# Kernel tuning notes

Measured on AMD Instinct MI355X. Metric: run time of the kernel, lower is better.

Reference implementation:

```python
import jax, jax.numpy as jnp
import numpy as np

ALPHA = 0.2  # LeakyReLU negative slope (init arg `alpha`)
N, F_IN, F_OUT = 8192, 512, 256


def setup_inputs() -> dict:
    key = jax.random.key(0)
    k1, k2, k3, k4 = jax.random.split(key, 4)
    x = jax.random.normal(k1, (N, F_IN), dtype=jnp.float32)
    adj = jax.random.randint(k2, (N, N), 0, 2, dtype=jnp.int32)
    W = jax.random.normal(k3, (F_IN, F_OUT), dtype=jnp.float32) * (1.0 / np.sqrt(F_IN))
    a = jax.random.normal(k4, (2 * F_OUT, 1), dtype=jnp.float32) * (1.0 / np.sqrt(F_IN))
    return {"x": x, "adj": adj, "W": W, "a": a}


def reference(x, adj, W, a):
    h = x @ W  # [N, F_OUT]
    f_out = W.shape[1]
    # e[i,j] = LeakyReLU(a1 . h_i + a2 . h_j); computed without the O(N^2*2F) concat
    f1 = h @ a[:f_out, 0]   # [N]
    f2 = h @ a[f_out:, 0]   # [N]
    s = f1[:, None] + f2[None, :]  # [N, N]
    e = jnp.where(s >= 0, s, ALPHA * s)
    # Faithful to the source bug: -9e15 * zeros_like == zeros, so masked entries are 0.0
    att = jnp.where(adj > 0, e, jnp.zeros((), dtype=e.dtype))
    att = jax.nn.softmax(att, axis=1)
    # dropout is identity in eval mode
    h_prime = att @ h  # [N, F_OUT]
    return jax.nn.elu(h_prime)  # concat=True branch
```

## Files before the change

### kernel.cpp

```cpp
#include <hip/hip_runtime.h>
#include <stdint.h>

#define NN 8192
#define FIN 512
#define FOUT 256
#define ALPHA 0.2f
#define KSPLIT 4

typedef float f32x4 __attribute__((ext_vector_type(4)));
typedef short s16x8 __attribute__((ext_vector_type(8)));

__device__ __forceinline__ uint16_t f2bf(float f) {
  union { float f; uint32_t u; } v; v.f = f;
  uint32_t u = v.u + 0x7fffu + ((v.u >> 16) & 1u);
  return (uint16_t)(u >> 16);
}

__global__ __launch_bounds__(256) void k_wa(const float* __restrict__ W,
                                            const float* __restrict__ a,
                                            float* __restrict__ wa1, float* __restrict__ wa2) {
  __shared__ float a1[256], a2[256];
  int tid = threadIdx.x;
  a1[tid] = a[tid];
  a2[tid] = a[tid + 256];
  __syncthreads();
  int m = blockIdx.x * 256 + tid;
  const float* wrow = W + (size_t)m * FOUT;
  float s1 = 0.f, s2 = 0.f;
  for (int k = 0; k < FOUT; k += 4) {
    f32x4 v = *(const f32x4*)(wrow + k);
#pragma unroll
    for (int i = 0; i < 4; i++) {
      s1 += v[i] * a1[k + i];
      s2 += v[i] * a2[k + i];
    }
  }
  wa1[m] = s1; wa2[m] = s2;
}

__global__ __launch_bounds__(256) void k_f1f2(const float* __restrict__ x,
                                              const float* __restrict__ wa1,
                                              const float* __restrict__ wa2,
                                              float* __restrict__ f1, float* __restrict__ f2) {
  __shared__ float s1[512], s2[512];
  int tid = threadIdx.x;
  s1[tid] = wa1[tid]; s1[tid + 256] = wa1[tid + 256];
  s2[tid] = wa2[tid]; s2[tid + 256] = wa2[tid + 256];
  __syncthreads();
  int w = tid >> 6, l = tid & 63;
  int row = blockIdx.x * 4 + w;
  const float* xr = x + (size_t)row * FIN + l * 8;
  f32x4 v0 = *(const f32x4*)xr;
  f32x4 v1 = *(const f32x4*)(xr + 4);
  int kb = l * 8;
  float d1 = 0.f, d2 = 0.f;
#pragma unroll
  for (int i = 0; i < 4; i++) {
    d1 += v0[i] * s1[kb + i] + v1[i] * s1[kb + 4 + i];
    d2 += v0[i] * s2[kb + i] + v1[i] * s2[kb + 4 + i];
  }
#pragma unroll
  for (int off = 32; off; off >>= 1) {
    d1 += __shfl_down(d1, off);
    d2 += __shfl_down(d2, off);
  }
  if (l == 0) { f1[row] = d1; f2[row] = d2; }
}

__global__ __launch_bounds__(256) void k_prep_wt(const float* __restrict__ W,
                                                 uint16_t* __restrict__ wt) {
  int idx = blockIdx.x * 256 + threadIdx.x;
  int f  = idx >> 7;
  int k4 = (idx & 127) * 4;
  ushort4 o;
  o.x = f2bf(W[(size_t)(k4 + 0) * FOUT + f]);
  o.y = f2bf(W[(size_t)(k4 + 1) * FOUT + f]);
  o.z = f2bf(W[(size_t)(k4 + 2) * FOUT + f]);
  o.w = f2bf(W[(size_t)(k4 + 3) * FOUT + f]);
  *(ushort4*)(wt + (size_t)f * FIN + k4) = o;
}

__global__ __launch_bounds__(256, 2) void k_gemm_h(const float* __restrict__ x,
                                                   const uint16_t* __restrict__ wt,
                                                   uint16_t* __restrict__ h) {
  __shared__ uint16_t Xs[64][40];
  __shared__ uint16_t Ws[128][40];
  int i0 = blockIdx.x * 64;
  int f0 = blockIdx.y * 128;
  int tid = threadIdx.x;
  int w = tid >> 6, l = tid & 63;
  int wr = w >> 1, wc = w & 1;
  int q = l >> 4, r16 = l & 15;
  f32x4 acc[2][4];
#pragma unroll
  for (int a = 0; a < 2; a++)
#pragma unroll
    for (int b = 0; b < 4; b++) acc[a][b] = (f32x4)0.f;

  int srow = tid >> 2, sch = tid & 3;
  for (int k0 = 0; k0 < FIN; k0 += 32) {
    const float* xp = x + (size_t)(i0 + srow) * FIN + k0 + sch * 8;
    f32x4 u0 = *(const f32x4*)xp;
    f32x4 u1 = *(const f32x4*)(xp + 4);
    uint4 pk;
    pk.x = (uint32_t)f2bf(u0[0]) | ((uint32_t)f2bf(u0[1]) << 16);
    pk.y = (uint32_t)f2bf(u0[2]) | ((uint32_t)f2bf(u0[3]) << 16);
    pk.z = (uint32_t)f2bf(u1[0]) | ((uint32_t)f2bf(u1[1]) << 16);
    pk.w = (uint32_t)f2bf(u1[2]) | ((uint32_t)f2bf(u1[3]) << 16);
    *(uint4*)(&Xs[srow][sch * 8]) = pk;
#pragma unroll
    for (int r = 0; r < 2; r++) {
      int idx = tid + r * 256;
      int rr = idx >> 2, cc = idx & 3;
      uint4 vw = *(const uint4*)(wt + (size_t)(f0 + rr) * FIN + k0 + cc * 8);
      *(uint4*)(&Ws[rr][cc * 8]) = vw;
    }
    __syncthreads();
    s16x8 A[2], B[4];
#pragma unroll
    for (int a = 0; a < 2; a++) A[a] = *(const s16x8*)(&Xs[wr * 32 + a * 16 + r16][q * 8]);
#pragma unroll
    for (int b = 0; b < 4; b++) B[b] = *(const s16x8*)(&Ws[wc * 64 + b * 16 + r16][q * 8]);
#pragma unroll
    for (int a = 0; a < 2; a++)
#pragma unroll
      for (int b = 0; b < 4; b++)
        acc[a][b] = __builtin_amdgcn_mfma_f32_16x16x32_bf16(A[a], B[b], acc[a][b], 0, 0, 0);
    __syncthreads();
  }
#pragma unroll
  for (int a = 0; a < 2; a++)
#pragma unroll
    for (int b = 0; b < 4; b++)
#pragma unroll
      for (int reg = 0; reg < 4; reg++) {
        int row = i0 + wr * 32 + a * 16 + q * 4 + reg;
        int col = f0 + wc * 64 + b * 16 + r16;
        h[(size_t)row * FOUT + col] = f2bf(acc[a][b][reg]);
      }
}

__global__ __launch_bounds__(256) void k_transpose(const uint16_t* __restrict__ h,
                                                   uint16_t* __restrict__ ht) {
  __shared__ uint16_t T[64][72];
  int i0 = blockIdx.x * 64, f0 = blockIdx.y * 64;
  int tid = threadIdx.x;
#pragma unroll
  for (int p = 0; p < 2; p++) {
    int idx = tid + p * 256;
    int r = idx >> 3, c8 = idx & 7;
    uint4 v = *(const uint4*)(h + (size_t)(i0 + r) * FOUT + f0 + c8 * 8);
    *(uint4*)(&T[r][c8 * 8]) = v;
  }
  __syncthreads();
#pragma unroll
  for (int p = 0; p < 2; p++) {
    int idx = tid + p * 256;
    int fr = idx >> 3, ic8 = idx & 7;
    s16x8 v;
#pragma unroll
    for (int j = 0; j < 8; j++) v[j] = (short)T[ic8 * 8 + j][fr];
    *(s16x8*)(ht + (size_t)(f0 + fr) * NN + i0 + ic8 * 8) = v;
  }
}

__global__ __launch_bounds__(256) void k_zero(float* __restrict__ l_arr) {
  l_arr[blockIdx.x * 256 + threadIdx.x] = 0.f;
}

__global__ __launch_bounds__(256, 2) void k_att(const int* __restrict__ adj,
                                                const uint16_t* __restrict__ ht,
                                                const float* __restrict__ f1,
                                                const float* __restrict__ f2,
                                                float* __restrict__ l_arr,
                                                float* __restrict__ part) {
  __shared__ uint16_t Ps[64][40];
  __shared__ uint16_t Hs[256][40];
  int i0 = blockIdx.x * 64;
  int jbase = blockIdx.y * (NN / KSPLIT);
  int tid = threadIdx.x;
  int w = tid >> 6, l = tid & 63;
  int q = l >> 4, r16 = l & 15;
  int prow = tid >> 2, pch = tid & 3;
  float f1i = f1[i0 + prow];
  float lsum = 0.f;
  f32x4 acc[4][4];
#pragma unroll
  for (int a = 0; a < 4; a++)
#pragma unroll
    for (int b = 0; b < 4; b++) acc[a][b] = (f32x4)0.f;

  for (int s = 0; s < NN / KSPLIT; s += 32) {
    int j0 = jbase + s;
#pragma unroll
    for (int p = 0; p < 4; p++) {
      int idx = tid + p * 256;
      int hr = idx >> 2, hc = idx & 3;
      uint4 v = *(const uint4*)(ht + (size_t)hr * NN + j0 + hc * 8);
      *(uint4*)(&Hs[hr][hc * 8]) = v;
    }
    const int* ap = adj + (size_t)(i0 + prow) * NN + j0 + pch * 8;
    int4 A0 = *(const int4*)ap;
    int4 A1 = *(const int4*)(ap + 4);
    f32x4 F0 = *(const f32x4*)(f2 + j0 + pch * 8);
    f32x4 F1 = *(const f32x4*)(f2 + j0 + pch * 8 + 4);
    s16x8 pv;
#define PCOMP(Ac, Fc, kk) { float s_ = f1i + (Fc); float e_ = s_ > 0.f ? s_ : ALPHA * s_; \
                            float p_ = ((Ac) != 0) ? __expf(e_) : 1.0f; lsum += p_; \
                            pv[kk] = (short)f2bf(p_); }
    PCOMP(A0.x, F0[0], 0); PCOMP(A0.y, F0[1], 1); PCOMP(A0.z, F0[2], 2); PCOMP(A0.w, F0[3], 3);
    PCOMP(A1.x, F1[0], 4); PCOMP(A1.y, F1[1], 5); PCOMP(A1.z, F1[2], 6); PCOMP(A1.w, F1[3], 7);
#undef PCOMP
    *(s16x8*)(&Ps[prow][pch * 8]) = pv;
    __syncthreads();

    s16x8 Af[4], Bf[4];
#pragma unroll
    for (int a = 0; a < 4; a++) Af[a] = *(const s16x8*)(&Ps[a * 16 + r16][q * 8]);
#pragma unroll
    for (int b = 0; b < 4; b++) Bf[b] = *(const s16x8*)(&Hs[w * 64 + b * 16 + r16][q * 8]);
#pragma unroll
    for (int a = 0; a < 4; a++)
#pragma unroll
      for (int b = 0; b < 4; b++)
        acc[a][b] = __builtin_amdgcn_mfma_f32_16x16x32_bf16(Af[a], Bf[b], acc[a][b], 0, 0, 0);
    __syncthreads();
  }

  lsum += __shfl_down(lsum, 2);
  lsum += __shfl_down(lsum, 1);
  if (pch == 0) atomicAdd(&l_arr[i0 + prow], lsum);

  float* pb = part + (size_t)blockIdx.y * ((size_t)NN * FOUT);
#pragma unroll
  for (int a = 0; a < 4; a++)
#pragma unroll
    for (int b = 0; b < 4; b++)
#pragma unroll
      for (int reg = 0; reg < 4; reg++) {
        int row = i0 + a * 16 + q * 4 + reg;
        int col = w * 64 + b * 16 + r16;
        pb[(size_t)row * FOUT + col] = acc[a][b][reg];
      }
}

__global__ __launch_bounds__(256) void k_combine(const float* __restrict__ part,
                                                 const float* __restrict__ l_arr,
                                                 float* __restrict__ out) {
  int idx = (blockIdx.x * 256 + threadIdx.x) * 4;
  float r = 1.0f / l_arr[idx >> 8];
  f32x4 v0 = *(const f32x4*)(part + 0 * (size_t)(NN * FOUT) + idx);
  f32x4 v1 = *(const f32x4*)(part + 1 * (size_t)(NN * FOUT) + idx);
  f32x4 v2 = *(const f32x4*)(part + 2 * (size_t)(NN * FOUT) + idx);
  f32x4 v3 = *(const f32x4*)(part + 3 * (size_t)(NN * FOUT) + idx);
  f32x4 o;
#pragma unroll
  for (int i = 0; i < 4; i++) {
    float v = (v0[i] + v1[i] + v2[i] + v3[i]) * r;
    o[i] = v > 0.f ? v : (__expf(v) - 1.f);
  }
  *(f32x4*)(out + idx) = o;
}

extern "C" void kernel_launch(void* const* d_in, const int* in_sizes, int n_in,
                              void* d_out, int out_size, void* d_ws, size_t ws_size,
                              hipStream_t stream) {
  const float* x   = (const float*)d_in[0];
  const int*   adj = (const int*)d_in[1];
  const float* W   = (const float*)d_in[2];
  const float* a   = (const float*)d_in[3];
  float* out = (float*)d_out;

  char* ws = (char*)d_ws;
  float*    wa1   = (float*)ws;
  float*    wa2   = wa1 + 512;
  float*    f1    = wa2 + 512;
  float*    f2    = f1 + NN;
  float*    l_arr = f2 + NN;
  uint16_t* wt    = (uint16_t*)(l_arr + NN);
  uint16_t* h     = wt + (size_t)FOUT * FIN;
  uint16_t* ht    = h + (size_t)NN * FOUT;
  float*    part  = (float*)(ht + (size_t)NN * FOUT);

  k_wa<<<2, 256, 0, stream>>>(W, a, wa1, wa2);
  k_f1f2<<<NN / 4, 256, 0, stream>>>(x, wa1, wa2, f1, f2);
  k_prep_wt<<<128, 256, 0, stream>>>(W, wt);
  k_gemm_h<<<dim3(NN / 64, 2), 256, 0, stream>>>(x, wt, h);
  k_transpose<<<dim3(NN / 64, FOUT / 64), 256, 0, stream>>>(h, ht);
  k_zero<<<NN / 256, 256, 0, stream>>>(l_arr);
  k_att<<<dim3(NN / 64, KSPLIT), 256, 0, stream>>>(adj, ht, f1, f2, l_arr, part);
  k_combine<<<NN * FOUT / 1024, 256, 0, stream>>>(part, l_arr, out);
}
```

Baseline: 457.7 us.

## Precompute packed adjacency bitmask in a streaming pass before attention kernel

Adds a kernel that streams the int32 adjacency matrix with nontemporal loads and packs it into a 1-bit-per-entry mask. The attention kernel then reads one mask byte per eight columns instead of two 16-byte int loads, which reduces memory traffic inside the compute-heavy kernel. The cost is an extra full pass over adjacency plus mask writes and another launch, and it needs extra workspace space after the partial buffers.

```diff
diff --git a/kernel.cpp b/kernel.cpp
--- a/kernel.cpp
+++ b/kernel.cpp
@@ -9,6 +9,7 @@
 
 typedef float f32x4 __attribute__((ext_vector_type(4)));
 typedef short s16x8 __attribute__((ext_vector_type(8)));
+typedef uint32_t u32x4 __attribute__((ext_vector_type(4)));
 
 __device__ __forceinline__ uint16_t f2bf(float f) {
   union { float f; uint32_t u; } v; v.f = f;
@@ -168,7 +169,21 @@
   l_arr[blockIdx.x * 256 + threadIdx.x] = 0.f;
 }
 
-__global__ __launch_bounds__(256, 2) void k_att(const int* __restrict__ adj,
+__global__ __launch_bounds__(256) void k_mask(const int* __restrict__ adj,
+                                              uint32_t* __restrict__ mask) {
+  int gid = blockIdx.x * 256 + threadIdx.x;
+  const u32x4* p = (const u32x4*)adj + (size_t)gid * 8;
+  uint32_t m = 0;
+#pragma unroll
+  for (int c = 0; c < 8; c++) {
+    u32x4 v = __builtin_nontemporal_load(p + c);
+#pragma unroll
+    for (int k = 0; k < 4; k++) m |= (v[k] != 0u ? 1u : 0u) << (c * 4 + k);
+  }
+  mask[gid] = m;
+}
+
+__global__ __launch_bounds__(256, 2) void k_att(const uint8_t* __restrict__ maskb,
                                                 const uint16_t* __restrict__ ht,
                                                 const float* __restrict__ f1,
                                                 const float* __restrict__ f2,
@@ -183,6 +198,7 @@
   int q = l >> 4, r16 = l & 15;
   int prow = tid >> 2, pch = tid & 3;
   float f1i = f1[i0 + prow];
+  const uint8_t* mrow = maskb + (size_t)(i0 + prow) * (NN / 8);
   float lsum = 0.f;
   f32x4 acc[4][4];
 #pragma unroll
@@ -199,17 +215,17 @@
       uint4 v = *(const uint4*)(ht + (size_t)hr * NN + j0 + hc * 8);
       *(uint4*)(&Hs[hr][hc * 8]) = v;
     }
-    const int* ap = adj + (size_t)(i0 + prow) * NN + j0 + pch * 8;
-    int4 A0 = *(const int4*)ap;
-    int4 A1 = *(const int4*)(ap + 4);
+    uint32_t mb = mrow[(j0 >> 3) + pch];
     f32x4 F0 = *(const f32x4*)(f2 + j0 + pch * 8);
     f32x4 F1 = *(const f32x4*)(f2 + j0 + pch * 8 + 4);
     s16x8 pv;
-#define PCOMP(Ac, Fc, kk) { float s_ = f1i + (Fc); float e_ = s_ > 0.f ? s_ : ALPHA * s_; \
-                            float p_ = ((Ac) != 0) ? __expf(e_) : 1.0f; lsum += p_; \
-                            pv[kk] = (short)f2bf(p_); }
-    PCOMP(A0.x, F0[0], 0); PCOMP(A0.y, F0[1], 1); PCOMP(A0.z, F0[2], 2); PCOMP(A0.w, F0[3], 3);
-    PCOMP(A1.x, F1[0], 4); PCOMP(A1.y, F1[1], 5); PCOMP(A1.z, F1[2], 6); PCOMP(A1.w, F1[3], 7);
+#define PCOMP(bit, Fc, kk) { float s_ = f1i + (Fc); float e_ = s_ > 0.f ? s_ : ALPHA * s_; \
+                             float p_ = (bit) ? __expf(e_) : 1.0f; lsum += p_; \
+                             pv[kk] = (short)f2bf(p_); }
+    PCOMP(mb & 1u,   F0[0], 0); PCOMP(mb & 2u,   F0[1], 1);
+    PCOMP(mb & 4u,   F0[2], 2); PCOMP(mb & 8u,   F0[3], 3);
+    PCOMP(mb & 16u,  F1[0], 4); PCOMP(mb & 32u,  F1[1], 5);
+    PCOMP(mb & 64u,  F1[2], 6); PCOMP(mb & 128u, F1[3], 7);
 #undef PCOMP
     *(s16x8*)(&Ps[prow][pch * 8]) = pv;
     __syncthreads();
@@ -281,6 +297,7 @@
   uint16_t* h     = wt + (size_t)FOUT * FIN;
   uint16_t* ht    = h + (size_t)NN * FOUT;
   float*    part  = (float*)(ht + (size_t)NN * FOUT);
+  uint32_t* mask  = (uint32_t*)(part + (size_t)KSPLIT * NN * FOUT);
 
   k_wa<<<2, 256, 0, stream>>>(W, a, wa1, wa2);
   k_f1f2<<<NN / 4, 256, 0, stream>>>(x, wa1, wa2, f1, f2);
@@ -288,6 +305,7 @@
   k_gemm_h<<<dim3(NN / 64, 2), 256, 0, stream>>>(x, wt, h);
   k_transpose<<<dim3(NN / 64, FOUT / 64), 256, 0, stream>>>(h, ht);
   k_zero<<<NN / 256, 256, 0, stream>>>(l_arr);
-  k_att<<<dim3(NN / 64, KSPLIT), 256, 0, stream>>>(adj, ht, f1, f2, l_arr, part);
+  k_mask<<<NN * NN / 32 / 256, 256, 0, stream>>>(adj, mask);
+  k_att<<<dim3(NN / 64, KSPLIT), 256, 0, stream>>>((const uint8_t*)mask, ht, f1, f2, l_arr, part);
   k_combine<<<NN * FOUT / 1024, 256, 0, stream>>>(part, l_arr, out);
 }
```

New measurement: 526.2 us. 1.15x slower.

## Double attention K-tile to 64, prefetch H into registers, fold zeroing into f1f2

Applied to the files above, without the earlier changes.

Doubles the K step of the attention kernel from 32 to 64 columns, halving the number of syncthreads-bracketed iterations and issuing two MFMA chunks per tile. The H tile is loaded into registers before the P computation and written to shared memory afterwards, so global load latency overlaps with the exp/softmax arithmetic. The separate l_arr zeroing kernel is removed and its work folded into k_f1f2, saving one launch. Shared memory grows to roughly 46KB per block and register pressure rises from the eight held uint4 values, which may hurt occupancy at the declared two blocks per CU.

```diff
diff --git a/kernel.cpp b/kernel.cpp
--- a/kernel.cpp
+++ b/kernel.cpp
@@ -41,9 +41,11 @@
 __global__ __launch_bounds__(256) void k_f1f2(const float* __restrict__ x,
                                               const float* __restrict__ wa1,
                                               const float* __restrict__ wa2,
-                                              float* __restrict__ f1, float* __restrict__ f2) {
+                                              float* __restrict__ f1, float* __restrict__ f2,
+                                              float* __restrict__ l_arr) {
   __shared__ float s1[512], s2[512];
   int tid = threadIdx.x;
+  if (tid < 4) l_arr[blockIdx.x * 4 + tid] = 0.f;
   s1[tid] = wa1[tid]; s1[tid + 256] = wa1[tid + 256];
   s2[tid] = wa2[tid]; s2[tid + 256] = wa2[tid + 256];
   __syncthreads();
@@ -164,24 +166,21 @@
   }
 }
 
-__global__ __launch_bounds__(256) void k_zero(float* __restrict__ l_arr) {
-  l_arr[blockIdx.x * 256 + threadIdx.x] = 0.f;
-}
-
 __global__ __launch_bounds__(256, 2) void k_att(const int* __restrict__ adj,
                                                 const uint16_t* __restrict__ ht,
                                                 const float* __restrict__ f1,
                                                 const float* __restrict__ f2,
                                                 float* __restrict__ l_arr,
                                                 float* __restrict__ part) {
-  __shared__ uint16_t Ps[64][40];
-  __shared__ uint16_t Hs[256][40];
+  __shared__ uint16_t Ps[64][72];
+  __shared__ uint16_t Hs[256][72];
   int i0 = blockIdx.x * 64;
   int jbase = blockIdx.y * (NN / KSPLIT);
   int tid = threadIdx.x;
   int w = tid >> 6, l = tid & 63;
   int q = l >> 4, r16 = l & 15;
   int prow = tid >> 2, pch = tid & 3;
+  int srow = tid >> 3, sch = tid & 7;
   float f1i = f1[i0 + prow];
   float lsum = 0.f;
   f32x4 acc[4][4];
@@ -190,40 +189,53 @@
 #pragma unroll
     for (int b = 0; b < 4; b++) acc[a][b] = (f32x4)0.f;
 
-  for (int s = 0; s < NN / KSPLIT; s += 32) {
+  for (int s = 0; s < NN / KSPLIT; s += 64) {
     int j0 = jbase + s;
-#pragma unroll
-    for (int p = 0; p < 4; p++) {
-      int idx = tid + p * 256;
-      int hr = idx >> 2, hc = idx & 3;
-      uint4 v = *(const uint4*)(ht + (size_t)hr * NN + j0 + hc * 8);
-      *(uint4*)(&Hs[hr][hc * 8]) = v;
-    }
-    const int* ap = adj + (size_t)(i0 + prow) * NN + j0 + pch * 8;
+    uint4 hv[8];
+#pragma unroll
+    for (int p = 0; p < 8; p++)
+      hv[p] = *(const uint4*)(ht + (size_t)(p * 32 + srow) * NN + j0 + sch * 8);
+    const int* ap = adj + (size_t)(i0 + prow) * NN + j0 + pch * 16;
     int4 A0 = *(const int4*)ap;
     int4 A1 = *(const int4*)(ap + 4);
-    f32x4 F0 = *(const f32x4*)(f2 + j0 + pch * 8);
-    f32x4 F1 = *(const f32x4*)(f2 + j0 + pch * 8 + 4);
-    s16x8 pv;
-#define PCOMP(Ac, Fc, kk) { float s_ = f1i + (Fc); float e_ = s_ > 0.f ? s_ : ALPHA * s_; \
-                            float p_ = ((Ac) != 0) ? __expf(e_) : 1.0f; lsum += p_; \
-                            pv[kk] = (short)f2bf(p_); }
-    PCOMP(A0.x, F0[0], 0); PCOMP(A0.y, F0[1], 1); PCOMP(A0.z, F0[2], 2); PCOMP(A0.w, F0[3], 3);
-    PCOMP(A1.x, F1[0], 4); PCOMP(A1.y, F1[1], 5); PCOMP(A1.z, F1[2], 6); PCOMP(A1.w, F1[3], 7);
+    int4 A2 = *(const int4*)(ap + 8);
+    int4 A3 = *(const int4*)(ap + 12);
+    f32x4 F0 = *(const f32x4*)(f2 + j0 + pch * 16);
+    f32x4 F1 = *(const f32x4*)(f2 + j0 + pch * 16 + 4);
+    f32x4 F2 = *(const f32x4*)(f2 + j0 + pch * 16 + 8);
+    f32x4 F3 = *(const f32x4*)(f2 + j0 + pch * 16 + 12);
+    s16x8 pv0, pv1;
+#define PCOMP(dst, Ac, Fc, kk) { float s_ = f1i + (Fc); float e_ = s_ > 0.f ? s_ : ALPHA * s_; \
+                                 float p_ = ((Ac) != 0) ? __expf(e_) : 1.0f; lsum += p_; \
+                                 dst[kk] = (short)f2bf(p_); }
+    PCOMP(pv0, A0.x, F0[0], 0); PCOMP(pv0, A0.y, F0[1], 1);
+    PCOMP(pv0, A0.z, F0[2], 2); PCOMP(pv0, A0.w, F0[3], 3);
+    PCOMP(pv0, A1.x, F1[0], 4); PCOMP(pv0, A1.y, F1[1], 5);
+    PCOMP(pv0, A1.z, F1[2], 6); PCOMP(pv0, A1.w, F1[3], 7);
+    PCOMP(pv1, A2.x, F2[0], 0); PCOMP(pv1, A2.y, F2[1], 1);
+    PCOMP(pv1, A2.z, F2[2], 2); PCOMP(pv1, A2.w, F2[3], 3);
+    PCOMP(pv1, A3.x, F3[0], 4); PCOMP(pv1, A3.y, F3[1], 5);
+    PCOMP(pv1, A3.z, F3[2], 6); PCOMP(pv1, A3.w, F3[3], 7);
 #undef PCOMP
-    *(s16x8*)(&Ps[prow][pch * 8]) = pv;
+    *(s16x8*)(&Ps[prow][pch * 16]) = pv0;
+    *(s16x8*)(&Ps[prow][pch * 16 + 8]) = pv1;
+#pragma unroll
+    for (int p = 0; p < 8; p++)
+      *(uint4*)(&Hs[p * 32 + srow][sch * 8]) = hv[p];
     __syncthreads();
-
-    s16x8 Af[4], Bf[4];
-#pragma unroll
-    for (int a = 0; a < 4; a++) Af[a] = *(const s16x8*)(&Ps[a * 16 + r16][q * 8]);
-#pragma unroll
-    for (int b = 0; b < 4; b++) Bf[b] = *(const s16x8*)(&Hs[w * 64 + b * 16 + r16][q * 8]);
-#pragma unroll
-    for (int a = 0; a < 4; a++)
-#pragma unroll
-      for (int b = 0; b < 4; b++)
-        acc[a][b] = __builtin_amdgcn_mfma_f32_16x16x32_bf16(Af[a], Bf[b], acc[a][b], 0, 0, 0);
+#pragma unroll
+    for (int c = 0; c < 2; c++) {
+      s16x8 Af[4], Bf[4];
+#pragma unroll
+      for (int a = 0; a < 4; a++) Af[a] = *(const s16x8*)(&Ps[a * 16 + r16][c * 32 + q * 8]);
+#pragma unroll
+      for (int b = 0; b < 4; b++) Bf[b] = *(const s16x8*)(&Hs[w * 64 + b * 16 + r16][c * 32 + q * 8]);
+#pragma unroll
+      for (int a = 0; a < 4; a++)
+#pragma unroll
+        for (int b = 0; b < 4; b++)
+          acc[a][b] = __builtin_amdgcn_mfma_f32_16x16x32_bf16(Af[a], Bf[b], acc[a][b], 0, 0, 0);
+    }
     __syncthreads();
   }
 
@@ -283,11 +295,10 @@
   float*    part  = (float*)(ht + (size_t)NN * FOUT);
 
   k_wa<<<2, 256, 0, stream>>>(W, a, wa1, wa2);
-  k_f1f2<<<NN / 4, 256, 0, stream>>>(x, wa1, wa2, f1, f2);
+  k_f1f2<<<NN / 4, 256, 0, stream>>>(x, wa1, wa2, f1, f2, l_arr);
   k_prep_wt<<<128, 256, 0, stream>>>(W, wt);
   k_gemm_h<<<dim3(NN / 64, 2), 256, 0, stream>>>(x, wt, h);
   k_transpose<<<dim3(NN / 64, FOUT / 64), 256, 0, stream>>>(h, ht);
-  k_zero<<<NN / 256, 256, 0, stream>>>(l_arr);
   k_att<<<dim3(NN / 64, KSPLIT), 256, 0, stream>>>(adj, ht, f1, f2, l_arr, part);
   k_combine<<<NN * FOUT / 1024, 256, 0, stream>>>(part, l_arr, out);
 }
```

After: 448.7 us. About the same (-2.0%).
